# Performance work log

Hardware: AMD Instinct MI355X
Metric: run time of the kernel (lower is better)

## Reference

```python
import jax, jax.numpy as jnp
import numpy as np

BLOCK = 512  # circulant block size

def block_circulant_matmul(x, w):
    """Block-circulant linear layer (CirCNN-style), no bias.
    x: (..., p*BLOCK); w: (q, p, BLOCK) -> out: (..., q*BLOCK).
    Each (q,p) block is a circulant matrix applied via FFT (circular conv).
    """
    q, p, b = w.shape
    xb = x.reshape(x.shape[:-1] + (p, b))            # (..., p, b)
    Xf = jnp.fft.rfft(xb, axis=-1)                    # (..., p, b//2+1) complex
    Wf = jnp.fft.rfft(w, axis=-1)                     # (q, p, b//2+1)
    Yf = jnp.einsum('...pf,qpf->...qf', Xf, Wf)       # sum over input blocks
    y = jnp.fft.irfft(Yf, n=b, axis=-1)               # (..., q, b)
    return y.reshape(x.shape[:-1] + (q * b,))

def setup_inputs() -> dict:
    key = jax.random.key(0)
    k1, k2, k3, k4 = jax.random.split(key, 4)
    d_model, d_ff, b = 2048, 5632, BLOCK
    p_in, q_ff = d_model // b, d_ff // b              # 4, 11
    scale = 1.0 / np.sqrt(d_model)
    x = jax.random.normal(k1, (4, 4096, d_model), dtype=jnp.float32)
    w_gate = jax.random.normal(k2, (q_ff, p_in, b), dtype=jnp.float32) * scale
    w_up   = jax.random.normal(k3, (q_ff, p_in, b), dtype=jnp.float32) * scale
    w_down = jax.random.normal(k4, (p_in, q_ff, b), dtype=jnp.float32) * (1.0 / np.sqrt(d_ff))
    return {"x": x, "w_gate": w_gate, "w_up": w_up, "w_down": w_down}

def reference(x, w_gate, w_up, w_down):
    # SwiGLU: down( SiLU(gate(x)) * up(x) ); dropout=0 -> identity
    gate = jax.nn.silu(block_circulant_matmul(x, w_gate))
    up = block_circulant_matmul(x, w_up)
    return block_circulant_matmul(gate * up, w_down)
```

## Files before the change

kernel.cpp:

```cpp
#include <hip/hip_runtime.h>
#include <math.h>


#define WAVE_FENCE() do { asm volatile("s_waitcnt lgkmcnt(0)" ::: "memory"); \
                          __builtin_amdgcn_sched_barrier(0); } while (0)

__device__ __forceinline__ int swz(int n) { return n ^ ((n >> 3) & 15); }

struct Tw { float t0r[7], t0i[7], t1r[7], t1i[7]; };

__device__ __forceinline__ void make_tw(int l, Tw& T)
{
    float c0, s0;
    __sincosf(-6.283185307179586f * (float)l * (1.0f/512.0f), &s0, &c0);
    float pr = c0, pi = s0;
    T.t0r[0] = pr; T.t0i[0] = pi;
#pragma unroll
    for (int m = 1; m < 7; ++m) {
        float nr = pr*c0 - pi*s0, ni = pr*s0 + pi*c0;
        pr = nr; pi = ni;
        T.t0r[m] = pr; T.t0i[m] = pi;
    }
    float c1, s1;
    __sincosf(-6.283185307179586f * (float)(l >> 3) * (1.0f/64.0f), &s1, &c1);
    pr = c1; pi = s1;
    T.t1r[0] = pr; T.t1i[0] = pi;
#pragma unroll
    for (int m = 1; m < 7; ++m) {
        float nr = pr*c1 - pi*s1, ni = pr*s1 + pi*c1;
        pr = nr; pi = ni;
        T.t1r[m] = pr; T.t1i[m] = pi;
    }
}

template<bool INV>
__device__ __forceinline__ void dft8(float xr[8], float xi[8])
{
    const float C = 0.70710678118654752f;
    float tr[4], ti[4], ur[4], ui[4];
#pragma unroll
    for (int q = 0; q < 4; ++q) {
        tr[q] = xr[q] + xr[q+4];  ti[q] = xi[q] + xi[q+4];
        ur[q] = xr[q] - xr[q+4];  ui[q] = xi[q] - xi[q+4];
    }
    {
        float xx = ur[1], yy = ui[1];
        if (!INV) { ur[1] = C*(xx+yy); ui[1] = C*(yy-xx); }
        else      { ur[1] = C*(xx-yy); ui[1] = C*(xx+yy); }
    }
    {
        float xx = ur[2], yy = ui[2];
        if (!INV) { ur[2] = yy;  ui[2] = -xx; }
        else      { ur[2] = -yy; ui[2] = xx; }
    }
    {
        float xx = ur[3], yy = ui[3];
        if (!INV) { ur[3] = C*(yy-xx);  ui[3] = -C*(xx+yy); }
        else      { ur[3] = -C*(xx+yy); ui[3] = C*(xx-yy); }
    }
    {
        float s0r=tr[0]+tr[2], s0i=ti[0]+ti[2];
        float d0r=tr[0]-tr[2], d0i=ti[0]-ti[2];
        float s1r=tr[1]+tr[3], s1i=ti[1]+ti[3];
        float e1r=tr[1]-tr[3], e1i=ti[1]-ti[3];
        float d1r, d1i;
        if (!INV) { d1r = e1i;  d1i = -e1r; } else { d1r = -e1i; d1i = e1r; }
        xr[0]=s0r+s1r; xi[0]=s0i+s1i;
        xr[2]=d0r+d1r; xi[2]=d0i+d1i;
        xr[4]=s0r-s1r; xi[4]=s0i-s1i;
        xr[6]=d0r-d1r; xi[6]=d0i-d1i;
    }
    {
        float s0r=ur[0]+ur[2], s0i=ui[0]+ui[2];
        float d0r=ur[0]-ur[2], d0i=ui[0]-ui[2];
        float s1r=ur[1]+ur[3], s1i=ui[1]+ui[3];
        float e1r=ur[1]-ur[3], e1i=ui[1]-ui[3];
        float d1r, d1i;
        if (!INV) { d1r = e1i;  d1i = -e1r; } else { d1r = -e1i; d1i = e1r; }
        xr[1]=s0r+s1r; xi[1]=s0i+s1i;
        xr[3]=d0r+d1r; xi[3]=d0i+d1i;
        xr[5]=s0r-s1r; xi[5]=s0i-s1i;
        xr[7]=d0r-d1r; xi[7]=d0i-d1i;
    }
}

template<bool INV>
__device__ __forceinline__ void fft512_r8(float2* wk, int l, const Tw& T)
{
    float xr[8], xi[8];
#pragma unroll
    for (int q = 0; q < 8; ++q) { float2 v = wk[swz(l + 64*q)]; xr[q]=v.x; xi[q]=v.y; }
    WAVE_FENCE();
    dft8<INV>(xr, xi);
#pragma unroll
    for (int m = 1; m < 8; ++m) {
        float wr = T.t0r[m-1], wi = INV ? -T.t0i[m-1] : T.t0i[m-1];
        float nr = xr[m]*wr - xi[m]*wi, ni = xr[m]*wi + xi[m]*wr;
        xr[m]=nr; xi[m]=ni;
    }
#pragma unroll
    for (int m = 0; m < 8; ++m) wk[swz(8*l + m)] = make_float2(xr[m], xi[m]);
    WAVE_FENCE();
#pragma unroll
    for (int q = 0; q < 8; ++q) { float2 v = wk[swz(l + 64*q)]; xr[q]=v.x; xi[q]=v.y; }
    WAVE_FENCE();
    dft8<INV>(xr, xi);
#pragma unroll
    for (int m = 1; m < 8; ++m) {
        float wr = T.t1r[m-1], wi = INV ? -T.t1i[m-1] : T.t1i[m-1];
        float nr = xr[m]*wr - xi[m]*wi, ni = xr[m]*wi + xi[m]*wr;
        xr[m]=nr; xi[m]=ni;
    }
    {
        const int base = 64*(l>>3) + (l&7);
#pragma unroll
        for (int m = 0; m < 8; ++m) wk[swz(base + 8*m)] = make_float2(xr[m], xi[m]);
    }
    WAVE_FENCE();
#pragma unroll
    for (int q = 0; q < 8; ++q) { float2 v = wk[swz(l + 64*q)]; xr[q]=v.x; xi[q]=v.y; }
    WAVE_FENCE();
    dft8<INV>(xr, xi);
#pragma unroll
    for (int m = 0; m < 8; ++m) wk[swz(l + 64*m)] = make_float2(xr[m], xi[m]);
    WAVE_FENCE();
}

__global__ __launch_bounds__(64) void wf_prep(const float* __restrict__ wg,
                                              const float* __restrict__ wu,
                                              const float* __restrict__ wd,
                                              float2* __restrict__ wsp)
{
    __shared__ float2 wk[512];
    const int t = threadIdx.x;
    Tw T; make_tw(t, T);
    const int b = blockIdx.x;
    const float* src = (b < 44) ? (wg + (size_t)b * 512)
                     : (b < 88) ? (wu + (size_t)(b - 44) * 512)
                                : (wd + (size_t)(b - 88) * 512);
    float2* dst = wsp + (size_t)b * 257;

#pragma unroll
    for (int i = 0; i < 8; ++i) { int n = t + 64*i; wk[swz(n)] = make_float2(src[n], 0.f); }
    WAVE_FENCE();
    fft512_r8<false>(wk, t, T);
    const float sc = 1.0f / 512.0f;
#pragma unroll
    for (int i = 0; i < 5; ++i) {
        int k = t + 64*i;
        if (k <= 256) { float2 z = wk[swz(k)]; dst[k] = make_float2(sc*z.x, sc*z.y); }
    }
}

__global__ __launch_bounds__(256) void bcffn(const float* __restrict__ x,
                                             const float2* __restrict__ wsp,
                                             float* __restrict__ out)
{
    __shared__ float2 sWork[4 * 512];
    __shared__ float2 sXf[4][257];
    __shared__ float2 sHf[11][257];

    const int tid = threadIdx.x;
    const int t = tid & 63, w = tid >> 6;
    const size_t row = blockIdx.x;

    Tw T; make_tw(t, T);

    const float2* Wg = wsp;
    const float2* Wu = wsp + 44 * 257;
    const float2* Wd = wsp + 88 * 257;

    float2* wk = sWork + (w << 9);

    {
        const float4* x4 = (const float4*)(x + row * 2048 + (size_t)w * 512);
#pragma unroll
        for (int u = 0; u < 2; ++u) {
            int e = t + 64*u;
            float4 a = x4[e];
            int n = 4*e;
            wk[swz(n+0)] = make_float2(a.x, 0.f);
            wk[swz(n+1)] = make_float2(a.y, 0.f);
            wk[swz(n+2)] = make_float2(a.z, 0.f);
            wk[swz(n+3)] = make_float2(a.w, 0.f);
        }
    }
    WAVE_FENCE();
    fft512_r8<false>(wk, t, T);
#pragma unroll
    for (int u = 0; u < 5; ++u) {
        int k = t + 64*u;
        if (k <= 256) sXf[w][k] = wk[swz(k)];
    }
    __syncthreads();

#pragma unroll 1
    for (int r = 0; r < 3; ++r) {
        const int q = r * 4 + w;
        if (q < 11) {
#pragma unroll
            for (int u = 0; u < 5; ++u) {
                int k = t + 64*u;
                if (k <= 256) {
                    float gr=0.f, gi=0.f, ur_=0.f, ui_=0.f;
#pragma unroll
                    for (int p = 0; p < 4; ++p) {
                        float2 X = sXf[p][k];
                        float2 a = Wg[(q*4 + p)*257 + k];
                        float2 b = Wu[(q*4 + p)*257 + k];
                        gr  += X.x*a.x - X.y*a.y;  gi  += X.x*a.y + X.y*a.x;
                        ur_ += X.x*b.x - X.y*b.y;  ui_ += X.x*b.y + X.y*b.x;
                    }
                    wk[swz(k)] = make_float2(gr - ui_, gi + ur_);
                    if (k != 0 && k != 256)
                        wk[swz(512 - k)] = make_float2(gr + ui_, ur_ - gi);
                }
            }
            WAVE_FENCE();
            fft512_r8<true>(wk, t, T);
#pragma unroll
            for (int u = 0; u < 8; ++u) {
                int n = t + 64*u;
                float2 v = wk[swz(n)];
                float h = v.x * v.y / (1.f + __expf(-v.x));
                wk[swz(n)] = make_float2(h, 0.f);
            }
            WAVE_FENCE();
            fft512_r8<false>(wk, t, T);
#pragma unroll
            for (int u = 0; u < 5; ++u) {
                int k = t + 64*u;
                if (k <= 256) sHf[q][k] = wk[swz(k)];
            }
            WAVE_FENCE();
        }
    }
    __syncthreads();

#pragma unroll
    for (int u = 0; u < 5; ++u) {
        int k = t + 64*u;
        if (k <= 256) {
            float zr = 0.f, zi = 0.f;
#pragma unroll
            for (int q = 0; q < 11; ++q) {
                float2 H = sHf[q][k];
                float2 d = Wd[(w*11 + q)*257 + k];
                zr += H.x*d.x - H.y*d.y;
                zi += H.x*d.y + H.y*d.x;
            }
            wk[swz(k)] = make_float2(zr, zi);
            if (k != 0 && k != 256)
                wk[swz(512 - k)] = make_float2(zr, -zi);
        }
    }
    WAVE_FENCE();
    fft512_r8<true>(wk, t, T);
    {
        float4* o4 = (float4*)(out + row * 2048 + (size_t)w * 512);
#pragma unroll
        for (int u = 0; u < 2; ++u) {
            int e = t + 64*u;
            int n = 4*e;
            o4[e] = make_float4(wk[swz(n)].x, wk[swz(n+1)].x,
                                wk[swz(n+2)].x, wk[swz(n+3)].x);
        }
    }
}

extern "C" void kernel_launch(void* const* d_in, const int* in_sizes, int n_in,
                              void* d_out, int out_size, void* d_ws, size_t ws_size,
                              hipStream_t stream)
{
    (void)n_in; (void)out_size; (void)ws_size;
    const float* x  = (const float*)d_in[0];
    const float* wg = (const float*)d_in[1];
    const float* wu = (const float*)d_in[2];
    const float* wd = (const float*)d_in[3];
    float2* wsp = (float2*)d_ws;
    float*  out = (float*)d_out;

    const int rows = in_sizes[0] / 2048;

    wf_prep<<<132, 64, 0, stream>>>(wg, wu, wd, wsp);
    bcffn<<<rows, 256, 0, stream>>>(x, wsp, out);
}
```

Before: 583.8 us.

## Accumulate down-projection spectra via LDS atomics and drop wave fences

Replaces the per-q hidden spectrum buffer (11x257 complex) with direct accumulation of the down-projection products into four shared accumulators using LDS float atomicAdd, shrinking shared memory and possibly raising occupancy. It also removes all explicit wave fences (s_waitcnt plus sched_barrier) between LDS writes and reads inside the FFT stages. The fence removal relies on the compiler inserting waits for intra-wave LDS dependencies, which it generally does. The atomics add contention and make the float summation order nondeterministic. The zero-initialization of the accumulators is not followed by a barrier before the atomics, though the earlier __syncthreads after the X FFT covers it.

```diff
diff --git a/kernel.cpp b/kernel.cpp
--- a/kernel.cpp
+++ b/kernel.cpp
@@ -1,9 +1,6 @@
 #include <hip/hip_runtime.h>
 #include <math.h>
 
-
-#define WAVE_FENCE() do { asm volatile("s_waitcnt lgkmcnt(0)" ::: "memory"); \
-                          __builtin_amdgcn_sched_barrier(0); } while (0)
 
 __device__ __forceinline__ int swz(int n) { return n ^ ((n >> 3) & 15); }
 
@@ -90,7 +87,6 @@
     float xr[8], xi[8];
 #pragma unroll
     for (int q = 0; q < 8; ++q) { float2 v = wk[swz(l + 64*q)]; xr[q]=v.x; xi[q]=v.y; }
-    WAVE_FENCE();
     dft8<INV>(xr, xi);
 #pragma unroll
     for (int m = 1; m < 8; ++m) {
@@ -100,10 +96,8 @@
     }
 #pragma unroll
     for (int m = 0; m < 8; ++m) wk[swz(8*l + m)] = make_float2(xr[m], xi[m]);
-    WAVE_FENCE();
 #pragma unroll
     for (int q = 0; q < 8; ++q) { float2 v = wk[swz(l + 64*q)]; xr[q]=v.x; xi[q]=v.y; }
-    WAVE_FENCE();
     dft8<INV>(xr, xi);
 #pragma unroll
     for (int m = 1; m < 8; ++m) {
@@ -116,14 +110,11 @@
 #pragma unroll
         for (int m = 0; m < 8; ++m) wk[swz(base + 8*m)] = make_float2(xr[m], xi[m]);
     }
-    WAVE_FENCE();
 #pragma unroll
     for (int q = 0; q < 8; ++q) { float2 v = wk[swz(l + 64*q)]; xr[q]=v.x; xi[q]=v.y; }
-    WAVE_FENCE();
     dft8<INV>(xr, xi);
 #pragma unroll
     for (int m = 0; m < 8; ++m) wk[swz(l + 64*m)] = make_float2(xr[m], xi[m]);
-    WAVE_FENCE();
 }
 
 __global__ __launch_bounds__(64) void wf_prep(const float* __restrict__ wg,
@@ -142,7 +133,6 @@
 
 #pragma unroll
     for (int i = 0; i < 8; ++i) { int n = t + 64*i; wk[swz(n)] = make_float2(src[n], 0.f); }
-    WAVE_FENCE();
     fft512_r8<false>(wk, t, T);
     const float sc = 1.0f / 512.0f;
 #pragma unroll
@@ -158,13 +148,16 @@
 {
     __shared__ float2 sWork[4 * 512];
     __shared__ float2 sXf[4][257];
-    __shared__ float2 sHf[11][257];
+    __shared__ float  sZr[4 * 257];
+    __shared__ float  sZi[4 * 257];
 
     const int tid = threadIdx.x;
     const int t = tid & 63, w = tid >> 6;
     const size_t row = blockIdx.x;
 
     Tw T; make_tw(t, T);
+
+    for (int i = tid; i < 1028; i += 256) { sZr[i] = 0.f; sZi[i] = 0.f; }
 
     const float2* Wg = wsp;
     const float2* Wu = wsp + 44 * 257;
@@ -185,7 +178,6 @@
             wk[swz(n+3)] = make_float2(a.w, 0.f);
         }
     }
-    WAVE_FENCE();
     fft512_r8<false>(wk, t, T);
 #pragma unroll
     for (int u = 0; u < 5; ++u) {
@@ -216,7 +208,6 @@
                         wk[swz(512 - k)] = make_float2(gr + ui_, ur_ - gi);
                 }
             }
-            WAVE_FENCE();
             fft512_r8<true>(wk, t, T);
 #pragma unroll
             for (int u = 0; u < 8; ++u) {
@@ -225,14 +216,20 @@
                 float h = v.x * v.y / (1.f + __expf(-v.x));
                 wk[swz(n)] = make_float2(h, 0.f);
             }
-            WAVE_FENCE();
             fft512_r8<false>(wk, t, T);
 #pragma unroll
             for (int u = 0; u < 5; ++u) {
                 int k = t + 64*u;
-                if (k <= 256) sHf[q][k] = wk[swz(k)];
+                if (k <= 256) {
+                    float2 H = wk[swz(k)];
+#pragma unroll
+                    for (int p = 0; p < 4; ++p) {
+                        float2 d = Wd[(p*11 + q)*257 + k];
+                        atomicAdd(&sZr[p*257 + k], H.x*d.x - H.y*d.y);
+                        atomicAdd(&sZi[p*257 + k], H.x*d.y + H.y*d.x);
+                    }
+                }
             }
-            WAVE_FENCE();
         }
     }
     __syncthreads();
@@ -241,20 +238,12 @@
     for (int u = 0; u < 5; ++u) {
         int k = t + 64*u;
         if (k <= 256) {
-            float zr = 0.f, zi = 0.f;
-#pragma unroll
-            for (int q = 0; q < 11; ++q) {
-                float2 H = sHf[q][k];
-                float2 d = Wd[(w*11 + q)*257 + k];
-                zr += H.x*d.x - H.y*d.y;
-                zi += H.x*d.y + H.y*d.x;
-            }
+            float zr = sZr[w*257 + k], zi = sZi[w*257 + k];
             wk[swz(k)] = make_float2(zr, zi);
             if (k != 0 && k != 256)
                 wk[swz(512 - k)] = make_float2(zr, -zi);
         }
     }
-    WAVE_FENCE();
     fft512_r8<true>(wk, t, T);
     {
         float4* o4 = (float4*)(out + row * 2048 + (size_t)w * 512);
```

Result: slower. 2.210 ms (+278.5%).

## Accumulate down-projection per round to shrink shared hidden-spectrum buffer

Applied to the files above, without the earlier changes.

The hidden spectra buffer shrinks from 11 to 4 slots. After each round of up to four hidden blocks (one per wave), the down-projection partial products are accumulated into per-thread registers, with a block barrier on each side. This cuts shared memory per block, which may allow more resident blocks per CU. In exchange it adds two block-wide syncs per round and five more live accumulator pairs per thread.

```diff
diff --git a/kernel.cpp b/kernel.cpp
--- a/kernel.cpp
+++ b/kernel.cpp
@@ -158,7 +158,7 @@
 {
     __shared__ float2 sWork[4 * 512];
     __shared__ float2 sXf[4][257];
-    __shared__ float2 sHf[11][257];
+    __shared__ float2 sHf[4][257];
 
     const int tid = threadIdx.x;
     const int t = tid & 63, w = tid >> 6;
@@ -171,6 +171,9 @@
     const float2* Wd = wsp + 88 * 257;
 
     float2* wk = sWork + (w << 9);
+
+    float Zr[5] = {0.f, 0.f, 0.f, 0.f, 0.f};
+    float Zi[5] = {0.f, 0.f, 0.f, 0.f, 0.f};
 
     {
         const float4* x4 = (const float4*)(x + row * 2048 + (size_t)w * 512);
@@ -230,28 +233,40 @@
 #pragma unroll
             for (int u = 0; u < 5; ++u) {
                 int k = t + 64*u;
-                if (k <= 256) sHf[q][k] = wk[swz(k)];
+                if (k <= 256) sHf[w][k] = wk[swz(k)];
             }
-            WAVE_FENCE();
-        }
-    }
-    __syncthreads();
+        }
+        __syncthreads();
+        {
+            const int nj = (r < 2) ? 4 : 3;
+#pragma unroll
+            for (int j = 0; j < 4; ++j) {
+                if (j < nj) {
+                    const int qq = r * 4 + j;
+                    const float2* wdq = Wd + (size_t)(w*11 + qq) * 257;
+#pragma unroll
+                    for (int u = 0; u < 5; ++u) {
+                        int k = t + 64*u;
+                        if (k <= 256) {
+                            float2 H = sHf[j][k];
+                            float2 d = wdq[k];
+                            Zr[u] += H.x*d.x - H.y*d.y;
+                            Zi[u] += H.x*d.y + H.y*d.x;
+                        }
+                    }
+                }
+            }
+        }
+        __syncthreads();
+    }
 
 #pragma unroll
     for (int u = 0; u < 5; ++u) {
         int k = t + 64*u;
         if (k <= 256) {
-            float zr = 0.f, zi = 0.f;
-#pragma unroll
-            for (int q = 0; q < 11; ++q) {
-                float2 H = sHf[q][k];
-                float2 d = Wd[(w*11 + q)*257 + k];
-                zr += H.x*d.x - H.y*d.y;
-                zi += H.x*d.y + H.y*d.x;
-            }
-            wk[swz(k)] = make_float2(zr, zi);
+            wk[swz(k)] = make_float2(Zr[u], Zi[u]);
             if (k != 0 && k != 256)
-                wk[swz(512 - k)] = make_float2(zr, -zi);
+                wk[swz(512 - k)] = make_float2(Zr[u], -Zi[u]);
         }
     }
     WAVE_FENCE();
```

New measurement: 668.4 us. 1.14x slower.

## Pack pairs of real FFTs into single complex FFTs across all stages

Applied to the files above, without the earlier changes.

Uses the two-for-one real FFT trick: the input transform packs two 512-blocks as real and imaginary parts, the hidden-state forward FFT packs two q blocks, and the output inverse FFT packs two output blocks whose spectra are combined through shared memory. This roughly halves the number of 512-point FFTs each row block performs. In exchange, some waves sit idle during the input and output stages, an extra __syncthreads is added, and there is extra split/merge arithmetic plus register storage for the intermediate hidden values.

```diff
diff --git a/kernel.cpp b/kernel.cpp
--- a/kernel.cpp
+++ b/kernel.cpp
@@ -172,71 +172,115 @@
 
     float2* wk = sWork + (w << 9);
 
-    {
-        const float4* x4 = (const float4*)(x + row * 2048 + (size_t)w * 512);
+    if (w < 2) {
+        const float4* xa = (const float4*)(x + row * 2048 + (size_t)(2*w)   * 512);
+        const float4* xb = (const float4*)(x + row * 2048 + (size_t)(2*w+1) * 512);
 #pragma unroll
         for (int u = 0; u < 2; ++u) {
             int e = t + 64*u;
-            float4 a = x4[e];
+            float4 a = xa[e], b = xb[e];
             int n = 4*e;
-            wk[swz(n+0)] = make_float2(a.x, 0.f);
-            wk[swz(n+1)] = make_float2(a.y, 0.f);
-            wk[swz(n+2)] = make_float2(a.z, 0.f);
-            wk[swz(n+3)] = make_float2(a.w, 0.f);
-        }
-    }
-    WAVE_FENCE();
-    fft512_r8<false>(wk, t, T);
-#pragma unroll
-    for (int u = 0; u < 5; ++u) {
-        int k = t + 64*u;
-        if (k <= 256) sXf[w][k] = wk[swz(k)];
+            wk[swz(n+0)] = make_float2(a.x, b.x);
+            wk[swz(n+1)] = make_float2(a.y, b.y);
+            wk[swz(n+2)] = make_float2(a.z, b.z);
+            wk[swz(n+3)] = make_float2(a.w, b.w);
+        }
+        WAVE_FENCE();
+        fft512_r8<false>(wk, t, T);
+#pragma unroll
+        for (int u = 0; u < 5; ++u) {
+            int k = t + 64*u;
+            if (k <= 256) {
+                float2 z = wk[swz(k)], m = wk[swz((512 - k) & 511)];
+                sXf[2*w][k]   = make_float2(0.5f*(z.x + m.x), 0.5f*(z.y - m.y));
+                sXf[2*w+1][k] = make_float2(0.5f*(z.y + m.y), 0.5f*(m.x - z.x));
+            }
+        }
     }
     __syncthreads();
 
-#pragma unroll 1
-    for (int r = 0; r < 3; ++r) {
-        const int q = r * 4 + w;
-        if (q < 11) {
-#pragma unroll
-            for (int u = 0; u < 5; ++u) {
-                int k = t + 64*u;
-                if (k <= 256) {
-                    float gr=0.f, gi=0.f, ur_=0.f, ui_=0.f;
-#pragma unroll
-                    for (int p = 0; p < 4; ++p) {
-                        float2 X = sXf[p][k];
-                        float2 a = Wg[(q*4 + p)*257 + k];
-                        float2 b = Wu[(q*4 + p)*257 + k];
-                        gr  += X.x*a.x - X.y*a.y;  gi  += X.x*a.y + X.y*a.x;
-                        ur_ += X.x*b.x - X.y*b.y;  ui_ += X.x*b.y + X.y*b.x;
-                    }
-                    wk[swz(k)] = make_float2(gr - ui_, gi + ur_);
-                    if (k != 0 && k != 256)
-                        wk[swz(512 - k)] = make_float2(gr + ui_, ur_ - gi);
+    auto einsum_gu = [&](int q) {
+#pragma unroll
+        for (int u = 0; u < 5; ++u) {
+            int k = t + 64*u;
+            if (k <= 256) {
+                float gr=0.f, gi=0.f, ur_=0.f, ui_=0.f;
+#pragma unroll
+                for (int p = 0; p < 4; ++p) {
+                    float2 X = sXf[p][k];
+                    float2 a = Wg[(q*4 + p)*257 + k];
+                    float2 b = Wu[(q*4 + p)*257 + k];
+                    gr  += X.x*a.x - X.y*a.y;  gi  += X.x*a.y + X.y*a.x;
+                    ur_ += X.x*b.x - X.y*b.y;  ui_ += X.x*b.y + X.y*b.x;
                 }
-            }
+                wk[swz(k)] = make_float2(gr - ui_, gi + ur_);
+                if (k != 0 && k != 256)
+                    wk[swz(512 - k)] = make_float2(gr + ui_, ur_ - gi);
+            }
+        }
+    };
+
+    {
+        const int qa = w, qb = w + 4;
+        float ha[8];
+
+        einsum_gu(qa);
+        WAVE_FENCE();
+        fft512_r8<true>(wk, t, T);
+#pragma unroll
+        for (int u = 0; u < 8; ++u) {
+            float2 v = wk[swz(t + 64*u)];
+            ha[u] = v.x * v.y / (1.f + __expf(-v.x));
+        }
+        WAVE_FENCE();
+
+        einsum_gu(qb);
+        WAVE_FENCE();
+        fft512_r8<true>(wk, t, T);
+#pragma unroll
+        for (int u = 0; u < 8; ++u) {
+            int n = t + 64*u;
+            float2 v = wk[swz(n)];
+            float hb = v.x * v.y / (1.f + __expf(-v.x));
+            wk[swz(n)] = make_float2(ha[u], hb);
+        }
+        WAVE_FENCE();
+        fft512_r8<false>(wk, t, T);
+#pragma unroll
+        for (int u = 0; u < 5; ++u) {
+            int k = t + 64*u;
+            if (k <= 256) {
+                float2 z = wk[swz(k)], m = wk[swz((512 - k) & 511)];
+                sHf[qa][k] = make_float2(0.5f*(z.x + m.x), 0.5f*(z.y - m.y));
+                sHf[qb][k] = make_float2(0.5f*(z.y + m.y), 0.5f*(m.x - z.x));
+            }
+        }
+        WAVE_FENCE();
+
+        if (w < 3) {
+            const int qc = w + 8;
+            einsum_gu(qc);
             WAVE_FENCE();
             fft512_r8<true>(wk, t, T);
 #pragma unroll
             for (int u = 0; u < 8; ++u) {
                 int n = t + 64*u;
                 float2 v = wk[swz(n)];
-                float h = v.x * v.y / (1.f + __expf(-v.x));
-                wk[swz(n)] = make_float2(h, 0.f);
+                wk[swz(n)] = make_float2(v.x * v.y / (1.f + __expf(-v.x)), 0.f);
             }
             WAVE_FENCE();
             fft512_r8<false>(wk, t, T);
 #pragma unroll
             for (int u = 0; u < 5; ++u) {
                 int k = t + 64*u;
-                if (k <= 256) sHf[q][k] = wk[swz(k)];
-            }
-            WAVE_FENCE();
+                if (k <= 256) sHf[qc][k] = wk[swz(k)];
+            }
         }
     }
     __syncthreads();
 
+    float Zr[5] = {0.f,0.f,0.f,0.f,0.f};
+    float Zi[5] = {0.f,0.f,0.f,0.f,0.f};
 #pragma unroll
     for (int u = 0; u < 5; ++u) {
         int k = t + 64*u;
@@ -249,21 +293,39 @@
                 zr += H.x*d.x - H.y*d.y;
                 zi += H.x*d.y + H.y*d.x;
             }
-            wk[swz(k)] = make_float2(zr, zi);
-            if (k != 0 && k != 256)
-                wk[swz(512 - k)] = make_float2(zr, -zi);
-        }
-    }
-    WAVE_FENCE();
-    fft512_r8<true>(wk, t, T);
-    {
-        float4* o4 = (float4*)(out + row * 2048 + (size_t)w * 512);
+            Zr[u] = zr; Zi[u] = zi;
+        }
+    }
+    if (w >= 2) {
+#pragma unroll
+        for (int u = 0; u < 5; ++u) {
+            int k = t + 64*u;
+            if (k <= 256) sXf[w-2][k] = make_float2(Zr[u], Zi[u]);
+        }
+    }
+    __syncthreads();
+    if (w < 2) {
+#pragma unroll
+        for (int u = 0; u < 5; ++u) {
+            int k = t + 64*u;
+            if (k <= 256) {
+                float2 zb = sXf[w][k];
+                wk[swz(k)] = make_float2(Zr[u] - zb.y, Zi[u] + zb.x);
+                if (k != 0 && k != 256)
+                    wk[swz(512 - k)] = make_float2(Zr[u] + zb.y, zb.x - Zi[u]);
+            }
+        }
+        WAVE_FENCE();
+        fft512_r8<true>(wk, t, T);
+        float4* oa = (float4*)(out + row * 2048 + (size_t)w       * 512);
+        float4* ob = (float4*)(out + row * 2048 + (size_t)(w + 2) * 512);
 #pragma unroll
         for (int u = 0; u < 2; ++u) {
-            int e = t + 64*u;
-            int n = 4*e;
-            o4[e] = make_float4(wk[swz(n)].x, wk[swz(n+1)].x,
-                                wk[swz(n+2)].x, wk[swz(n+3)].x);
+            int e = t + 64*u, n = 4*e;
+            float2 v0 = wk[swz(n)],   v1 = wk[swz(n+1)];
+            float2 v2 = wk[swz(n+2)], v3 = wk[swz(n+3)];
+            oa[e] = make_float4(v0.x, v1.x, v2.x, v3.x);
+            ob[e] = make_float4(v0.y, v1.y, v2.y, v3.y);
         }
     }
 }
```

Measured after the change: 579.6 us. No clear change (-0.7%).
